# Optimization experiments

Hardware: AMD Instinct MI355X
Metric: run time of the kernel (lower is better)

Reference implementation:

```python
import jax, jax.numpy as jnp
import numpy as np

NUM_EVENT = 50000
NUM_STATION = 5000
N = 8388608          # number of phase picks
NR, NZ = 512, 256    # eikonal grid
H = 0.5              # grid spacing (km)
RG0, ZG0 = 0.0, 0.0  # grid origins
VP, VS = 6.0, 6.0 / 1.73


def _bilin(tables, ptype, r, z):
    """Bilinear interpolation of stacked [2,NR,NZ] tables at (r,z), per-row table ptype."""
    fr = (r - RG0) / H
    fz = (z - ZG0) / H
    ir0 = jnp.clip(jnp.floor(fr), 0, NR - 2).astype(jnp.int32)
    iz0 = jnp.clip(jnp.floor(fz), 0, NZ - 2).astype(jnp.int32)
    x = fr - ir0
    y = fz - iz0
    Q00 = tables[ptype, ir0, iz0]
    Q01 = tables[ptype, ir0, iz0 + 1]
    Q10 = tables[ptype, ir0 + 1, iz0]
    Q11 = tables[ptype, ir0 + 1, iz0 + 1]
    return Q00 * (1 - x) * (1 - y) + Q01 * (1 - x) * y + Q10 * x * (1 - y) + Q11 * x * y


def setup_inputs() -> dict:
    key = jax.random.key(0)
    ks = jax.random.split(key, 10)
    station_index = jax.random.randint(ks[0], (N,), 0, NUM_STATION)
    event_index = jax.random.randint(ks[1], (N,), 0, NUM_EVENT)
    phase_type = jax.random.randint(ks[2], (N,), 0, 2)
    phase_time = jax.random.uniform(ks[3], (N,), jnp.float32, 0.0, 60.0)
    phase_weight = jax.random.uniform(ks[4], (N,), jnp.float32, 0.0, 1.0)
    # embedding weights (event_loc/event_time trainable; station tables frozen)
    event_loc_w = jax.random.uniform(ks[5], (NUM_EVENT, 3), jnp.float32) * jnp.array([200.0, 200.0, 20.0], jnp.float32)
    event_time_w = jax.random.normal(ks[6], (NUM_EVENT, 1), jnp.float32)
    station_loc_w = jax.random.uniform(ks[7], (NUM_STATION, 3), jnp.float32) * jnp.array([200.0, 200.0, 2.0], jnp.float32)
    station_dt_w = 0.1 * jax.random.normal(ks[8], (NUM_STATION, 1), jnp.float32)
    # synthetic eikonal tables (smooth, physically plausible): tt = dist / v
    rg = jnp.arange(NR, dtype=jnp.float32) * H + RG0
    zg = jnp.arange(NZ, dtype=jnp.float32) * H + ZG0
    dist = jnp.sqrt(rg[:, None] ** 2 + zg[None, :] ** 2)
    safe = jnp.maximum(dist, 1e-6)
    tt_tables = jnp.stack([dist / VP, dist / VS])                 # [2,NR,NZ] P,S
    grad_r_tables = jnp.stack([rg[:, None] / safe / VP, rg[:, None] / safe / VS])
    grad_z_tables = jnp.stack([zg[None, :] / safe / VP, zg[None, :] / safe / VS])
    grad_r_tables = jnp.broadcast_to(grad_r_tables, (2, NR, NZ)).astype(jnp.float32)
    grad_z_tables = jnp.broadcast_to(grad_z_tables, (2, NR, NZ)).astype(jnp.float32)
    return {
        "station_index": station_index, "event_index": event_index, "phase_type": phase_type,
        "phase_time": phase_time, "phase_weight": phase_weight,
        "event_loc_w": event_loc_w, "event_time_w": event_time_w,
        "station_loc_w": station_loc_w, "station_dt_w": station_dt_w,
        "tt_tables": tt_tables, "grad_r_tables": grad_r_tables, "grad_z_tables": grad_z_tables,
    }


def reference(station_index, event_index, phase_type, phase_time, phase_weight,
              event_loc_w, event_time_w, station_loc_w, station_dt_w,
              tt_tables, grad_r_tables, grad_z_tables):
    ev = event_loc_w[event_index]        # [N,3]
    st = station_loc_w[station_index]    # [N,3]
    r = jnp.linalg.norm(ev[:, :2] - st[:, :2], axis=-1)  # epicentral distance
    z = ev[:, 2] - st[:, 2]                               # depth difference
    tt = _bilin(tt_tables, phase_type, r, z)              # eikonal travel time
    pred_time = event_time_w[event_index, 0] + tt + station_dt_w[station_index, 0]
    residual = phase_time - pred_time
    d = jnp.abs(residual)
    huber = jnp.where(d < 1.0, 0.5 * d * d, d - 0.5)      # F.huber_loss, delta=1
    loss = jnp.sum(huber * phase_weight)
    return pred_time, residual, loss
```

## Files before the change

kernel.cpp:

```cpp
#include <hip/hip_runtime.h>
#include <hip/hip_fp16.h>


constexpr int   kN   = 8388608;
constexpr int   kNR  = 512;
constexpr int   kNZ  = 256;
constexpr int   kNE  = 50000;
constexpr int   kNS  = 5000;
constexpr float kInvH = 2.0f;

constexpr int kIZV    = 41;
constexpr int kVROW   = kNR;
constexpr int kVPLANE = kIZV * kNR;
constexpr int kVERT   = 2 * kVPLANE;

typedef float nfloat4 __attribute__((ext_vector_type(4)));
typedef int   nint4   __attribute__((ext_vector_type(4)));

__device__ __forceinline__ unsigned pack2h(float a, float b) {
    __half2 h = __floats2half2_rn(a, b);
    return *reinterpret_cast<unsigned*>(&h);
}
__device__ __forceinline__ float2 unpack2h(unsigned u) {
    __half2 h = *reinterpret_cast<__half2*>(&u);
    return __half22float2(h);
}
__device__ __forceinline__ void nt_store4(float* p, float a, float b, float c, float d) {
    nfloat4 v = { a, b, c, d };
    __builtin_nontemporal_store(v, reinterpret_cast<nfloat4*>(p));
}

__global__ void zero_loss_kernel(float* __restrict__ loss) {
    if (threadIdx.x == 0 && blockIdx.x == 0) *loss = 0.0f;
}

__global__ __launch_bounds__(256) void pack_kernel(
    const float* __restrict__ event_loc_w,
    const float* __restrict__ event_time_w,
    const float* __restrict__ station_loc_w,
    const float* __restrict__ station_dt_w,
    const float* __restrict__ tt_tables,
    uint2*  __restrict__ ev_h,
    uint2*  __restrict__ st_h,
    __half* __restrict__ vert_h,
    float*  __restrict__ loss_out)
{
    const int i = blockIdx.x * blockDim.x + threadIdx.x;
    if (i == 0) *loss_out = 0.0f;

    if (i < kNE) {
        ev_h[i] = make_uint2(pack2h(event_loc_w[i * 3 + 0], event_loc_w[i * 3 + 1]),
                             pack2h(event_loc_w[i * 3 + 2], event_time_w[i]));
    }
    if (i < kNS) {
        st_h[i] = make_uint2(pack2h(station_loc_w[i * 3 + 0], station_loc_w[i * 3 + 1]),
                             pack2h(station_loc_w[i * 3 + 2], station_dt_w[i]));
    }
    if (i < kVERT) {
        const int p  = i / kVPLANE;
        const int rm = i - p * kVPLANE;
        const int iz = rm >> 9;
        const int ir = rm & 511;
        vert_h[i] = __float2half(tt_tables[p * (kNR * kNZ) + ir * kNZ + iz]);
    }
}

__global__ __launch_bounds__(1024, 4) void travel_time_h_kernel(
    const int*    __restrict__ station_index,
    const int*    __restrict__ event_index,
    const int*    __restrict__ phase_type,
    const float*  __restrict__ phase_time,
    const float*  __restrict__ phase_weight,
    const uint2*  __restrict__ ev_h,
    const uint2*  __restrict__ st_h,
    const __half* __restrict__ vert_h,
    float* __restrict__ pred_out,
    float* __restrict__ resid_out,
    float* __restrict__ loss_out)
{
    __shared__ __align__(16) uint2  st_lds[kNS];
    __shared__ __align__(16) __half vert_lds[kVERT];
    __shared__ float wsum[16];

    const int tid   = threadIdx.x;
    const int baseA = blockIdx.x * 8192 + tid * 4;
    const int baseB = baseA + 4096;

    const nint4   siA = __builtin_nontemporal_load(reinterpret_cast<const nint4*>(station_index + baseA));
    const nint4   eiA = __builtin_nontemporal_load(reinterpret_cast<const nint4*>(event_index   + baseA));
    const nint4   ptA = __builtin_nontemporal_load(reinterpret_cast<const nint4*>(phase_type    + baseA));
    const nfloat4 tmA = __builtin_nontemporal_load(reinterpret_cast<const nfloat4*>(phase_time   + baseA));
    const nfloat4 pwA = __builtin_nontemporal_load(reinterpret_cast<const nfloat4*>(phase_weight + baseA));
    const nint4   siB = __builtin_nontemporal_load(reinterpret_cast<const nint4*>(station_index + baseB));
    const nint4   eiB = __builtin_nontemporal_load(reinterpret_cast<const nint4*>(event_index   + baseB));
    const nint4   ptB = __builtin_nontemporal_load(reinterpret_cast<const nint4*>(phase_type    + baseB));
    const nfloat4 tmB = __builtin_nontemporal_load(reinterpret_cast<const nfloat4*>(phase_time   + baseB));
    const nfloat4 pwB = __builtin_nontemporal_load(reinterpret_cast<const nfloat4*>(phase_weight + baseB));

    {
        const uint4* srcS = reinterpret_cast<const uint4*>(st_h);
        uint4*       dstS = reinterpret_cast<uint4*>(st_lds);
        for (int i = tid; i < 2500; i += 1024) dstS[i] = srcS[i];
        const uint4* srcV = reinterpret_cast<const uint4*>(vert_h);
        uint4*       dstV = reinterpret_cast<uint4*>(vert_lds);
        for (int i = tid; i < 5248; i += 1024) dstV[i] = srcV[i];
    }
    __syncthreads();

    const int eiAk[4] = { eiA.x, eiA.y, eiA.z, eiA.w };
    const int eiBk[4] = { eiB.x, eiB.y, eiB.z, eiB.w };
    const int siAk[4] = { siA.x, siA.y, siA.z, siA.w };
    const int siBk[4] = { siB.x, siB.y, siB.z, siB.w };
    const int ptAk[4] = { ptA.x, ptA.y, ptA.z, ptA.w };
    const int ptBk[4] = { ptB.x, ptB.y, ptB.z, ptB.w };
    const float tmAk[4] = { tmA.x, tmA.y, tmA.z, tmA.w };
    const float tmBk[4] = { tmB.x, tmB.y, tmB.z, tmB.w };
    const float pwAk[4] = { pwA.x, pwA.y, pwA.z, pwA.w };
    const float pwBk[4] = { pwB.x, pwB.y, pwB.z, pwB.w };

    uint2 eA[4], eB[4], sA[4], sB[4];
    #pragma unroll
    for (int k = 0; k < 4; ++k) eA[k] = ev_h[eiAk[k]];
    #pragma unroll
    for (int k = 0; k < 4; ++k) eB[k] = ev_h[eiBk[k]];
    #pragma unroll
    for (int k = 0; k < 4; ++k) sA[k] = st_lds[siAk[k]];
    #pragma unroll
    for (int k = 0; k < 4; ++k) sB[k] = st_lds[siBk[k]];

    float lsum = 0.0f;
    float predA[4], resA[4], predB[4], resB[4];

    #pragma unroll
    for (int k = 0; k < 4; ++k) {
        const float2 exy = unpack2h(eA[k].x);
        const float2 ezt = unpack2h(eA[k].y);
        const float2 sxy = unpack2h(sA[k].x);
        const float2 szt = unpack2h(sA[k].y);
        const float dx = exy.x - sxy.x;
        const float dy = exy.y - sxy.y;
        const float r  = sqrtf(dx * dx + dy * dy);
        const float z  = ezt.x - szt.x;
        const float fr = r * kInvH;
        const float fz = z * kInvH;
        const int ir0 = (int)fminf(fmaxf(floorf(fr), 0.0f), (float)(kNR - 2));
        const int iz0 = (int)fminf(fmaxf(floorf(fz), 0.0f), (float)(kIZV - 2));
        const float x = fr - (float)ir0;
        const float y = fz - (float)iz0;
        const int vb = ptAk[k] * kVPLANE + iz0 * kVROW + ir0;
        const float v00 = __half2float(vert_lds[vb]);
        const float v10 = __half2float(vert_lds[vb + 1]);
        const float v01 = __half2float(vert_lds[vb + kVROW]);
        const float v11 = __half2float(vert_lds[vb + kVROW + 1]);
        const float tt = v00 * (1.0f - x) * (1.0f - y)
                       + v01 * (1.0f - x) * y
                       + v10 * x * (1.0f - y)
                       + v11 * x * y;
        const float pt_ = ezt.y + tt + szt.y;
        const float rr  = tmAk[k] - pt_;
        predA[k] = pt_;
        resA[k]  = rr;
        const float d = fabsf(rr);
        lsum += ((d < 1.0f) ? 0.5f * d * d : d - 0.5f) * pwAk[k];
    }
    #pragma unroll
    for (int k = 0; k < 4; ++k) {
        const float2 exy = unpack2h(eB[k].x);
        const float2 ezt = unpack2h(eB[k].y);
        const float2 sxy = unpack2h(sB[k].x);
        const float2 szt = unpack2h(sB[k].y);
        const float dx = exy.x - sxy.x;
        const float dy = exy.y - sxy.y;
        const float r  = sqrtf(dx * dx + dy * dy);
        const float z  = ezt.x - szt.x;
        const float fr = r * kInvH;
        const float fz = z * kInvH;
        const int ir0 = (int)fminf(fmaxf(floorf(fr), 0.0f), (float)(kNR - 2));
        const int iz0 = (int)fminf(fmaxf(floorf(fz), 0.0f), (float)(kIZV - 2));
        const float x = fr - (float)ir0;
        const float y = fz - (float)iz0;
        const int vb = ptBk[k] * kVPLANE + iz0 * kVROW + ir0;
        const float v00 = __half2float(vert_lds[vb]);
        const float v10 = __half2float(vert_lds[vb + 1]);
        const float v01 = __half2float(vert_lds[vb + kVROW]);
        const float v11 = __half2float(vert_lds[vb + kVROW + 1]);
        const float tt = v00 * (1.0f - x) * (1.0f - y)
                       + v01 * (1.0f - x) * y
                       + v10 * x * (1.0f - y)
                       + v11 * x * y;
        const float pt_ = ezt.y + tt + szt.y;
        const float rr  = tmBk[k] - pt_;
        predB[k] = pt_;
        resB[k]  = rr;
        const float d = fabsf(rr);
        lsum += ((d < 1.0f) ? 0.5f * d * d : d - 0.5f) * pwBk[k];
    }

    nt_store4(pred_out  + baseA, predA[0], predA[1], predA[2], predA[3]);
    nt_store4(resid_out + baseA, resA[0],  resA[1],  resA[2],  resA[3]);
    nt_store4(pred_out  + baseB, predB[0], predB[1], predB[2], predB[3]);
    nt_store4(resid_out + baseB, resB[0],  resB[1],  resB[2],  resB[3]);

    #pragma unroll
    for (int off = 32; off > 0; off >>= 1)
        lsum += __shfl_down(lsum, off);

    const int lane = tid & 63;
    const int wid  = tid >> 6;
    if (lane == 0) wsum[wid] = lsum;
    __syncthreads();
    if (tid == 0) {
        float b = 0.0f;
        #pragma unroll
        for (int w = 0; w < 16; ++w) b += wsum[w];
        atomicAdd(loss_out, b);
    }
}

__global__ __launch_bounds__(256) void travel_time_kernel(
    const int*   __restrict__ station_index,
    const int*   __restrict__ event_index,
    const int*   __restrict__ phase_type,
    const float* __restrict__ phase_time,
    const float* __restrict__ phase_weight,
    const float* __restrict__ event_loc_w,
    const float* __restrict__ event_time_w,
    const float* __restrict__ station_loc_w,
    const float* __restrict__ station_dt_w,
    const float* __restrict__ tt_tables,
    float* __restrict__ pred_out,
    float* __restrict__ resid_out,
    float* __restrict__ loss_out)
{
    const int tid     = blockIdx.x * blockDim.x + threadIdx.x;
    const int nthread = gridDim.x * blockDim.x;
    float lsum = 0.0f;

    for (int base = tid * 4; base < kN; base += nthread * 4) {
        const int4   si4 = *reinterpret_cast<const int4*>(station_index + base);
        const int4   ei4 = *reinterpret_cast<const int4*>(event_index   + base);
        const int4   pt4 = *reinterpret_cast<const int4*>(phase_type    + base);
        const float4 tm4 = *reinterpret_cast<const float4*>(phase_time   + base);
        const float4 pw4 = *reinterpret_cast<const float4*>(phase_weight + base);
        const int   si[4] = { si4.x, si4.y, si4.z, si4.w };
        const int   ei[4] = { ei4.x, ei4.y, ei4.z, ei4.w };
        const int   pt[4] = { pt4.x, pt4.y, pt4.z, pt4.w };
        const float tm[4] = { tm4.x, tm4.y, tm4.z, tm4.w };
        const float pw[4] = { pw4.x, pw4.y, pw4.z, pw4.w };
        float pred[4], res[4];
        #pragma unroll
        for (int k = 0; k < 4; ++k) {
            const int e = ei[k], s = si[k], p = pt[k];
            const float dx = event_loc_w[e*3+0] - station_loc_w[s*3+0];
            const float dy = event_loc_w[e*3+1] - station_loc_w[s*3+1];
            const float r  = sqrtf(dx*dx + dy*dy);
            const float z  = event_loc_w[e*3+2] - station_loc_w[s*3+2];
            const float fr = r * kInvH, fz = z * kInvH;
            const int ir0 = (int)fminf(fmaxf(floorf(fr), 0.0f), (float)(kNR - 2));
            const int iz0 = (int)fminf(fmaxf(floorf(fz), 0.0f), (float)(kNZ - 2));
            const float x = fr - (float)ir0, y = fz - (float)iz0;
            const float* tb = tt_tables + (size_t)p * (kNR*kNZ) + ir0 * kNZ + iz0;
            const float tt = tb[0]*(1.0f-x)*(1.0f-y) + tb[1]*(1.0f-x)*y
                           + tb[kNZ]*x*(1.0f-y) + tb[kNZ+1]*x*y;
            const float pt_ = event_time_w[e] + tt + station_dt_w[s];
            const float rr  = tm[k] - pt_;
            pred[k] = pt_; res[k] = rr;
            const float d = fabsf(rr);
            lsum += ((d < 1.0f) ? 0.5f*d*d : d - 0.5f) * pw[k];
        }
        *reinterpret_cast<float4*>(pred_out  + base) = make_float4(pred[0], pred[1], pred[2], pred[3]);
        *reinterpret_cast<float4*>(resid_out + base) = make_float4(res[0],  res[1],  res[2],  res[3]);
    }
    #pragma unroll
    for (int off = 32; off > 0; off >>= 1) lsum += __shfl_down(lsum, off);
    __shared__ float wsum[4];
    if ((threadIdx.x & 63) == 0) wsum[threadIdx.x >> 6] = lsum;
    __syncthreads();
    if (threadIdx.x == 0) atomicAdd(loss_out, wsum[0]+wsum[1]+wsum[2]+wsum[3]);
}

extern "C" void kernel_launch(void* const* d_in, const int* in_sizes, int n_in,
                              void* d_out, int out_size, void* d_ws, size_t ws_size,
                              hipStream_t stream) {
    const int*   station_index = (const int*)  d_in[0];
    const int*   event_index   = (const int*)  d_in[1];
    const int*   phase_type    = (const int*)  d_in[2];
    const float* phase_time    = (const float*)d_in[3];
    const float* phase_weight  = (const float*)d_in[4];
    const float* event_loc_w   = (const float*)d_in[5];
    const float* event_time_w  = (const float*)d_in[6];
    const float* station_loc_w = (const float*)d_in[7];
    const float* station_dt_w  = (const float*)d_in[8];
    const float* tt_tables     = (const float*)d_in[9];

    float* out       = (float*)d_out;
    float* pred_out  = out;
    float* resid_out = out + kN;
    float* loss_out  = out + 2 * kN;

    const size_t ws_needed = (size_t)(kNE + kNS) * sizeof(uint2) + (size_t)kVERT * sizeof(__half);

    if (ws_size >= ws_needed) {
        uint2*  ev_h   = (uint2*)d_ws;
        uint2*  st_h   = ev_h + kNE;
        __half* vert_h = (__half*)(st_h + kNS);

        pack_kernel<<<196, 256, 0, stream>>>(
            event_loc_w, event_time_w, station_loc_w, station_dt_w, tt_tables,
            ev_h, st_h, vert_h, loss_out);

        travel_time_h_kernel<<<kN / 8192, 1024, 0, stream>>>(
            station_index, event_index, phase_type, phase_time, phase_weight,
            ev_h, st_h, vert_h, pred_out, resid_out, loss_out);
    } else {
        zero_loss_kernel<<<1, 64, 0, stream>>>(loss_out);
        travel_time_kernel<<<2048, 256, 0, stream>>>(
            station_index, event_index, phase_type, phase_time, phase_weight,
            event_loc_w, event_time_w, station_loc_w, station_dt_w, tt_tables,
            pred_out, resid_out, loss_out);
    }
}
```

Before: 77.99 us.

## Make travel-time blocks persistent over four chunks with software-pipelined loads

Launches 256 blocks of 1024 threads instead of 1024, and each block now handles four 8192-element chunks. Stream loads for later chunks are issued before computing earlier ones. This spreads the per-block LDS fill of the station and travel-time tables over four times more work and overlaps global loads with compute. In exchange it holds more registers per thread, drops the min-blocks launch bound, and with 256 blocks leaves less parallelism available to hide gather latency.

```diff
diff --git a/kernel.cpp b/kernel.cpp
--- a/kernel.cpp
+++ b/kernel.cpp
@@ -65,7 +65,112 @@
     }
 }
 
-__global__ __launch_bounds__(1024, 4) void travel_time_h_kernel(
+struct ChunkRegs {
+    nint4   si, ei, pt;
+    nfloat4 tm, pw;
+    nint4   si2, ei2, pt2;
+    nfloat4 tm2, pw2;
+    uint2   ev[8];
+};
+
+__device__ __forceinline__ void load_chunk(
+    int base,
+    const int* __restrict__ si_p, const int* __restrict__ ei_p,
+    const int* __restrict__ pt_p, const float* __restrict__ tm_p,
+    const float* __restrict__ pw_p, ChunkRegs& c)
+{
+    const int b2 = base + 4096;
+    c.si  = __builtin_nontemporal_load(reinterpret_cast<const nint4*>(si_p + base));
+    c.ei  = __builtin_nontemporal_load(reinterpret_cast<const nint4*>(ei_p + base));
+    c.pt  = __builtin_nontemporal_load(reinterpret_cast<const nint4*>(pt_p + base));
+    c.tm  = __builtin_nontemporal_load(reinterpret_cast<const nfloat4*>(tm_p + base));
+    c.pw  = __builtin_nontemporal_load(reinterpret_cast<const nfloat4*>(pw_p + base));
+    c.si2 = __builtin_nontemporal_load(reinterpret_cast<const nint4*>(si_p + b2));
+    c.ei2 = __builtin_nontemporal_load(reinterpret_cast<const nint4*>(ei_p + b2));
+    c.pt2 = __builtin_nontemporal_load(reinterpret_cast<const nint4*>(pt_p + b2));
+    c.tm2 = __builtin_nontemporal_load(reinterpret_cast<const nfloat4*>(tm_p + b2));
+    c.pw2 = __builtin_nontemporal_load(reinterpret_cast<const nfloat4*>(pw_p + b2));
+}
+
+__device__ __forceinline__ void gather_chunk(const uint2* __restrict__ ev_h, ChunkRegs& c)
+{
+    c.ev[0] = ev_h[c.ei.x];
+    c.ev[1] = ev_h[c.ei.y];
+    c.ev[2] = ev_h[c.ei.z];
+    c.ev[3] = ev_h[c.ei.w];
+    c.ev[4] = ev_h[c.ei2.x];
+    c.ev[5] = ev_h[c.ei2.y];
+    c.ev[6] = ev_h[c.ei2.z];
+    c.ev[7] = ev_h[c.ei2.w];
+}
+
+__device__ __forceinline__ float half_compute(
+    const nint4 si, const nint4 pt, const nfloat4 tm, const nfloat4 pw,
+    const uint2* __restrict__ evp,
+    const uint2* st_lds, const __half* vert_lds,
+    int base, float* __restrict__ pred_out, float* __restrict__ resid_out)
+{
+    const int   sik[4] = { si.x, si.y, si.z, si.w };
+    const int   ptk[4] = { pt.x, pt.y, pt.z, pt.w };
+    const float tmk[4] = { tm.x, tm.y, tm.z, tm.w };
+    const float pwk[4] = { pw.x, pw.y, pw.z, pw.w };
+
+    uint2 s[4];
+    #pragma unroll
+    for (int k = 0; k < 4; ++k) s[k] = st_lds[sik[k]];
+
+    float lsum = 0.0f;
+    float pred[4], res[4];
+    #pragma unroll
+    for (int k = 0; k < 4; ++k) {
+        const float2 exy = unpack2h(evp[k].x);
+        const float2 ezt = unpack2h(evp[k].y);
+        const float2 sxy = unpack2h(s[k].x);
+        const float2 szt = unpack2h(s[k].y);
+        const float dx = exy.x - sxy.x;
+        const float dy = exy.y - sxy.y;
+        const float r  = sqrtf(dx * dx + dy * dy);
+        const float z  = ezt.x - szt.x;
+        const float fr = r * kInvH;
+        const float fz = z * kInvH;
+        const int ir0 = (int)fminf(fmaxf(floorf(fr), 0.0f), (float)(kNR - 2));
+        const int iz0 = (int)fminf(fmaxf(floorf(fz), 0.0f), (float)(kIZV - 2));
+        const float x = fr - (float)ir0;
+        const float y = fz - (float)iz0;
+        const int vb = ptk[k] * kVPLANE + iz0 * kVROW + ir0;
+        const float v00 = __half2float(vert_lds[vb]);
+        const float v10 = __half2float(vert_lds[vb + 1]);
+        const float v01 = __half2float(vert_lds[vb + kVROW]);
+        const float v11 = __half2float(vert_lds[vb + kVROW + 1]);
+        const float tt = v00 * (1.0f - x) * (1.0f - y)
+                       + v01 * (1.0f - x) * y
+                       + v10 * x * (1.0f - y)
+                       + v11 * x * y;
+        const float pt_ = ezt.y + tt + szt.y;
+        const float rr  = tmk[k] - pt_;
+        pred[k] = pt_;
+        res[k]  = rr;
+        const float d = fabsf(rr);
+        lsum += ((d < 1.0f) ? 0.5f * d * d : d - 0.5f) * pwk[k];
+    }
+    nt_store4(pred_out  + base, pred[0], pred[1], pred[2], pred[3]);
+    nt_store4(resid_out + base, res[0],  res[1],  res[2],  res[3]);
+    return lsum;
+}
+
+__device__ __forceinline__ float compute_chunk(
+    const ChunkRegs& c, int base,
+    const uint2* st_lds, const __half* vert_lds,
+    float* __restrict__ pred_out, float* __restrict__ resid_out)
+{
+    float l = half_compute(c.si,  c.pt,  c.tm,  c.pw,  c.ev,     st_lds, vert_lds,
+                           base,        pred_out, resid_out);
+    l      += half_compute(c.si2, c.pt2, c.tm2, c.pw2, c.ev + 4, st_lds, vert_lds,
+                           base + 4096, pred_out, resid_out);
+    return l;
+}
+
+__global__ __launch_bounds__(1024) void travel_time_h_kernel(
     const int*    __restrict__ station_index,
     const int*    __restrict__ event_index,
     const int*    __restrict__ phase_type,
@@ -82,20 +187,12 @@
     __shared__ __align__(16) __half vert_lds[kVERT];
     __shared__ float wsum[16];
 
-    const int tid   = threadIdx.x;
-    const int baseA = blockIdx.x * 8192 + tid * 4;
-    const int baseB = baseA + 4096;
-
-    const nint4   siA = __builtin_nontemporal_load(reinterpret_cast<const nint4*>(station_index + baseA));
-    const nint4   eiA = __builtin_nontemporal_load(reinterpret_cast<const nint4*>(event_index   + baseA));
-    const nint4   ptA = __builtin_nontemporal_load(reinterpret_cast<const nint4*>(phase_type    + baseA));
-    const nfloat4 tmA = __builtin_nontemporal_load(reinterpret_cast<const nfloat4*>(phase_time   + baseA));
-    const nfloat4 pwA = __builtin_nontemporal_load(reinterpret_cast<const nfloat4*>(phase_weight + baseA));
-    const nint4   siB = __builtin_nontemporal_load(reinterpret_cast<const nint4*>(station_index + baseB));
-    const nint4   eiB = __builtin_nontemporal_load(reinterpret_cast<const nint4*>(event_index   + baseB));
-    const nint4   ptB = __builtin_nontemporal_load(reinterpret_cast<const nint4*>(phase_type    + baseB));
-    const nfloat4 tmB = __builtin_nontemporal_load(reinterpret_cast<const nfloat4*>(phase_time   + baseB));
-    const nfloat4 pwB = __builtin_nontemporal_load(reinterpret_cast<const nfloat4*>(phase_weight + baseB));
+    const int tid = threadIdx.x;
+
+    const int base0 = (blockIdx.x)            * 8192 + tid * 4;
+    const int base1 = (256  + (int)blockIdx.x) * 8192 + tid * 4;
+    const int base2 = (512  + (int)blockIdx.x) * 8192 + tid * 4;
+    const int base3 = (768  + (int)blockIdx.x) * 8192 + tid * 4;
 
     {
         const uint4* srcS = reinterpret_cast<const uint4*>(st_h);
@@ -105,101 +202,28 @@
         uint4*       dstV = reinterpret_cast<uint4*>(vert_lds);
         for (int i = tid; i < 5248; i += 1024) dstV[i] = srcV[i];
     }
+
+    ChunkRegs c0, c1, c2, c3;
+    load_chunk(base0, station_index, event_index, phase_type, phase_time, phase_weight, c0);
+    load_chunk(base1, station_index, event_index, phase_type, phase_time, phase_weight, c1);
+
     __syncthreads();
 
-    const int eiAk[4] = { eiA.x, eiA.y, eiA.z, eiA.w };
-    const int eiBk[4] = { eiB.x, eiB.y, eiB.z, eiB.w };
-    const int siAk[4] = { siA.x, siA.y, siA.z, siA.w };
-    const int siBk[4] = { siB.x, siB.y, siB.z, siB.w };
-    const int ptAk[4] = { ptA.x, ptA.y, ptA.z, ptA.w };
-    const int ptBk[4] = { ptB.x, ptB.y, ptB.z, ptB.w };
-    const float tmAk[4] = { tmA.x, tmA.y, tmA.z, tmA.w };
-    const float tmBk[4] = { tmB.x, tmB.y, tmB.z, tmB.w };
-    const float pwAk[4] = { pwA.x, pwA.y, pwA.z, pwA.w };
-    const float pwBk[4] = { pwB.x, pwB.y, pwB.z, pwB.w };
-
-    uint2 eA[4], eB[4], sA[4], sB[4];
-    #pragma unroll
-    for (int k = 0; k < 4; ++k) eA[k] = ev_h[eiAk[k]];
-    #pragma unroll
-    for (int k = 0; k < 4; ++k) eB[k] = ev_h[eiBk[k]];
-    #pragma unroll
-    for (int k = 0; k < 4; ++k) sA[k] = st_lds[siAk[k]];
-    #pragma unroll
-    for (int k = 0; k < 4; ++k) sB[k] = st_lds[siBk[k]];
-
     float lsum = 0.0f;
-    float predA[4], resA[4], predB[4], resB[4];
-
-    #pragma unroll
-    for (int k = 0; k < 4; ++k) {
-        const float2 exy = unpack2h(eA[k].x);
-        const float2 ezt = unpack2h(eA[k].y);
-        const float2 sxy = unpack2h(sA[k].x);
-        const float2 szt = unpack2h(sA[k].y);
-        const float dx = exy.x - sxy.x;
-        const float dy = exy.y - sxy.y;
-        const float r  = sqrtf(dx * dx + dy * dy);
-        const float z  = ezt.x - szt.x;
-        const float fr = r * kInvH;
-        const float fz = z * kInvH;
-        const int ir0 = (int)fminf(fmaxf(floorf(fr), 0.0f), (float)(kNR - 2));
-        const int iz0 = (int)fminf(fmaxf(floorf(fz), 0.0f), (float)(kIZV - 2));
-        const float x = fr - (float)ir0;
-        const float y = fz - (float)iz0;
-        const int vb = ptAk[k] * kVPLANE + iz0 * kVROW + ir0;
-        const float v00 = __half2float(vert_lds[vb]);
-        const float v10 = __half2float(vert_lds[vb + 1]);
-        const float v01 = __half2float(vert_lds[vb + kVROW]);
-        const float v11 = __half2float(vert_lds[vb + kVROW + 1]);
-        const float tt = v00 * (1.0f - x) * (1.0f - y)
-                       + v01 * (1.0f - x) * y
-                       + v10 * x * (1.0f - y)
-                       + v11 * x * y;
-        const float pt_ = ezt.y + tt + szt.y;
-        const float rr  = tmAk[k] - pt_;
-        predA[k] = pt_;
-        resA[k]  = rr;
-        const float d = fabsf(rr);
-        lsum += ((d < 1.0f) ? 0.5f * d * d : d - 0.5f) * pwAk[k];
-    }
-    #pragma unroll
-    for (int k = 0; k < 4; ++k) {
-        const float2 exy = unpack2h(eB[k].x);
-        const float2 ezt = unpack2h(eB[k].y);
-        const float2 sxy = unpack2h(sB[k].x);
-        const float2 szt = unpack2h(sB[k].y);
-        const float dx = exy.x - sxy.x;
-        const float dy = exy.y - sxy.y;
-        const float r  = sqrtf(dx * dx + dy * dy);
-        const float z  = ezt.x - szt.x;
-        const float fr = r * kInvH;
-        const float fz = z * kInvH;
-        const int ir0 = (int)fminf(fmaxf(floorf(fr), 0.0f), (float)(kNR - 2));
-        const int iz0 = (int)fminf(fmaxf(floorf(fz), 0.0f), (float)(kIZV - 2));
-        const float x = fr - (float)ir0;
-        const float y = fz - (float)iz0;
-        const int vb = ptBk[k] * kVPLANE + iz0 * kVROW + ir0;
-        const float v00 = __half2float(vert_lds[vb]);
-        const float v10 = __half2float(vert_lds[vb + 1]);
-        const float v01 = __half2float(vert_lds[vb + kVROW]);
-        const float v11 = __half2float(vert_lds[vb + kVROW + 1]);
-        const float tt = v00 * (1.0f - x) * (1.0f - y)
-                       + v01 * (1.0f - x) * y
-                       + v10 * x * (1.0f - y)
-                       + v11 * x * y;
-        const float pt_ = ezt.y + tt + szt.y;
-        const float rr  = tmBk[k] - pt_;
-        predB[k] = pt_;
-        resB[k]  = rr;
-        const float d = fabsf(rr);
-        lsum += ((d < 1.0f) ? 0.5f * d * d : d - 0.5f) * pwBk[k];
-    }
-
-    nt_store4(pred_out  + baseA, predA[0], predA[1], predA[2], predA[3]);
-    nt_store4(resid_out + baseA, resA[0],  resA[1],  resA[2],  resA[3]);
-    nt_store4(pred_out  + baseB, predB[0], predB[1], predB[2], predB[3]);
-    nt_store4(resid_out + baseB, resB[0],  resB[1],  resB[2],  resB[3]);
+
+    gather_chunk(ev_h, c0);
+    load_chunk(base2, station_index, event_index, phase_type, phase_time, phase_weight, c2);
+    lsum += compute_chunk(c0, base0, st_lds, vert_lds, pred_out, resid_out);
+
+    gather_chunk(ev_h, c1);
+    load_chunk(base3, station_index, event_index, phase_type, phase_time, phase_weight, c3);
+    lsum += compute_chunk(c1, base1, st_lds, vert_lds, pred_out, resid_out);
+
+    gather_chunk(ev_h, c2);
+    lsum += compute_chunk(c2, base2, st_lds, vert_lds, pred_out, resid_out);
+
+    gather_chunk(ev_h, c3);
+    lsum += compute_chunk(c3, base3, st_lds, vert_lds, pred_out, resid_out);
 
     #pragma unroll
     for (int off = 32; off > 0; off >>= 1)
@@ -309,7 +333,7 @@
             event_loc_w, event_time_w, station_loc_w, station_dt_w, tt_tables,
             ev_h, st_h, vert_h, loss_out);
 
-        travel_time_h_kernel<<<kN / 8192, 1024, 0, stream>>>(
+        travel_time_h_kernel<<<256, 1024, 0, stream>>>(
             station_index, event_index, phase_type, phase_time, phase_weight,
             ev_h, st_h, vert_h, pred_out, resid_out, loss_out);
     } else {
```

Measured after the change: 84.87 us. 8.8% more time.
